# Optimization experiments

Measured on AMD Instinct MI355X. Metric: run time of the kernel, lower is better.

## Reference

```python
import jax, jax.numpy as jnp
import numpy as np

NUM_VARS = 10
HID = 256
INP = 4
B = 32
T = 64

_adj = np.ones((NUM_VARS, NUM_VARS)) - np.eye(NUM_VARS)
SEND, RECV = np.where(_adj)          # each [E], E = num_vars*(num_vars-1) = 90
E = len(SEND)
_e2n = np.zeros((NUM_VARS, E), dtype=np.float32)
_e2n[RECV, np.arange(E)] = 1.0       # encode_onehot(recv).T -> [num_vars, E]
E2N = jnp.asarray(_e2n)
SEND_J = jnp.asarray(SEND)
RECV_J = jnp.asarray(RECV)


def _mlp_block(x, w1, b1, w2, b2, gamma, beta):
    # RefNRIMLP: elu(fc1) -> (dropout p=0) -> elu(fc2) -> batchnorm over view(-1, H)
    h = jax.nn.elu(x @ w1 + b1)
    h = jax.nn.elu(h @ w2 + b2)
    mu = h.mean(axis=(0, 1, 2), keepdims=True)
    var = h.var(axis=(0, 1, 2), keepdims=True)
    return gamma * (h - mu) * jax.lax.rsqrt(var + 1e-5) + beta


def setup_inputs() -> dict:
    key = jax.random.key(0)
    ks = jax.random.split(key, 12)

    def xavier(k, fi, fo):
        return jax.random.normal(k, (fi, fo), jnp.float32) * np.sqrt(2.0 / (fi + fo))

    d = {
        "x": jax.random.normal(ks[0], (B, T, NUM_VARS, INP), jnp.float32),
        # mlp1: inp -> hid -> hid
        "w1a": xavier(ks[1], INP, HID), "b1a": jnp.full((HID,), 0.1),
        "w1b": xavier(ks[2], HID, HID), "b1b": jnp.full((HID,), 0.1),
        "g1": jnp.ones((HID,)), "be1": jnp.zeros((HID,)),
        # mlp2: 2*hid -> hid -> hid
        "w2a": xavier(ks[3], 2 * HID, HID), "b2a": jnp.full((HID,), 0.1),
        "w2b": xavier(ks[4], HID, HID), "b2b": jnp.full((HID,), 0.1),
        "g2": jnp.ones((HID,)), "be2": jnp.zeros((HID,)),
        # mlp3: hid -> hid -> hid
        "w3a": xavier(ks[5], HID, HID), "b3a": jnp.full((HID,), 0.1),
        "w3b": xavier(ks[6], HID, HID), "b3b": jnp.full((HID,), 0.1),
        "g3": jnp.ones((HID,)), "be3": jnp.zeros((HID,)),
        # output heads
        "wo1": xavier(ks[7], HID, HID), "bo1": jnp.full((HID,), 0.1),
        "wo2": xavier(ks[8], HID, 1), "bo2": jnp.full((1,), 0.1),
    }
    return d


def reference(x, w1a, b1a, w1b, b1b, g1, be1,
              w2a, b2a, w2b, b2b, g2, be2,
              w3a, b3a, w3b, b3b, g3, be3,
              wo1, bo1, wo2, bo2):
    # x: [B, T, N, INP] -> transpose(2,1): [B, N, T, INP]
    h = jnp.transpose(x, (0, 2, 1, 3))
    h = _mlp_block(h, w1a, b1a, w1b, b1b, g1, be1)            # [B, N, T, H]
    # node2edge: gather senders/receivers along node dim, concat on features
    e = jnp.concatenate([h[:, SEND_J], h[:, RECV_J]], axis=-1)  # [B, E, T, 2H]
    e = _mlp_block(e, w2a, b2a, w2b, b2b, g2, be2)            # [B, E, T, H]
    # edge2node: incidence matmul over edge dim, normalize by in-degree
    n = jnp.einsum('ve,betH->bvtH', E2N, e) / (NUM_VARS - 1)   # [B, N, T, H]
    n = _mlp_block(n, w3a, b3a, w3b, b3b, g3, be3)
    n = jax.nn.relu(n) @ wo1 + bo1
    n = jax.nn.relu(n) @ wo2 + bo2                             # [B, N, T, 1]
    out = jnp.transpose(n, (0, 2, 1, 3)).mean(axis=-1)         # [B, T, N]
    return out
```

## Files before the change

### kernel.cpp

```cpp
#include <hip/hip_runtime.h>
#include <hip/hip_bf16.h>
#include <cstdint>

#define DI __device__ __forceinline__

typedef short bf16x8 __attribute__((ext_vector_type(8)));
typedef float f32x4 __attribute__((ext_vector_type(4)));
typedef unsigned short u16;
typedef unsigned short u16x8 __attribute__((ext_vector_type(8)));

static constexpr int NV = 10, NE = 90, TT = 64;
static constexpr int R1 = 20480;
static constexpr int R2 = 184320;

DI float bf2f(u16 u) { union { unsigned int i; float f; } x; x.i = ((unsigned int)u) << 16; return x.f; }
DI u16 f2bf(float f) { unsigned int u = __float_as_uint(f); return (u16)((u + 0x7FFF + ((u >> 16) & 1)) >> 16); }
DI float elu(float v) { return v > 0.f ? v : __expf(v) - 1.f; }

#define GLL(srcp, dstp) __builtin_amdgcn_global_load_lds( \
    (const __attribute__((address_space(1))) unsigned int*)(srcp), \
    (__attribute__((address_space(3))) unsigned int*)(dstp), 16, 0, 0)

__global__ __launch_bounds__(256) void pack4(
    const float* __restrict__ s0, u16* __restrict__ d0,
    const float* __restrict__ s1, u16* __restrict__ d1,
    const float* __restrict__ s2, u16* __restrict__ d2,
    const float* __restrict__ s3, u16* __restrict__ d3) {
    const float* s; u16* d;
    switch (blockIdx.y) {
        case 0: s = s0; d = d0; break;
        case 1: s = s1; d = d1; break;
        case 2: s = s2; d = d2; break;
        default: s = s3; d = d3; break;
    }
    int tid = threadIdx.x;
    int bn = blockIdx.x >> 3, kt = blockIdx.x & 7;
#pragma unroll
    for (int p = 0; p < 2; ++p) {
        int n = bn * 128 + p * 64 + (tid >> 2);
        int k = kt * 32 + (tid & 3) * 8;
        u16x8 pk;
#pragma unroll
        for (int e = 0; e < 8; ++e) pk[e] = f2bf(s[(size_t)(k + e) * 256 + n]);
        *(u16x8*)(d + ((size_t)((bn * 8 + kt) * 2 + p)) * 2048 + (size_t)tid * 8) = pk;
    }
}

__global__ __launch_bounds__(256) void pack256s(const float* __restrict__ s,
                                                u16* __restrict__ d) {
    int kt = blockIdx.x;
#pragma unroll
    for (int h = 0; h < 4; ++h) {
        int tid2 = threadIdx.x + h * 256;
        int n = tid2 >> 2;
        int g = (tid2 & 3) ^ ((tid2 >> 2) & 3);
        int k = kt * 32 + g * 8;
        u16x8 pk;
#pragma unroll
        for (int e = 0; e < 8; ++e) pk[e] = f2bf(s[(size_t)(k + e) * 256 + n]);
        *(u16x8*)(d + (size_t)kt * 8192 + (size_t)tid2 * 8) = pk;
    }
}

__global__ __launch_bounds__(256) void pack256s_w2a(const float* __restrict__ w2a,
                                                    const float* __restrict__ scsh1,
                                                    u16* __restrict__ d) {
    int kt = blockIdx.x;
#pragma unroll
    for (int h = 0; h < 4; ++h) {
        int tid2 = threadIdx.x + h * 256;
        int n = tid2 >> 2;
        int g = (tid2 & 3) ^ ((tid2 >> 2) & 3);
        int k = kt * 32 + g * 8;
        u16x8 pk;
#pragma unroll
        for (int e = 0; e < 8; ++e)
            pk[e] = f2bf(scsh1[(k + e) & 255] * w2a[(size_t)(k + e) * 256 + n]);
        *(u16x8*)(d + (size_t)kt * 8192 + (size_t)tid2 * 8) = pk;
    }
}

__global__ void zero_stats(float* p, int n) {
    int i = blockIdx.x * 256 + threadIdx.x;
    if (i < n) p[i] = 0.f;
}

__global__ void conv_wo2(const float* __restrict__ src, u16* __restrict__ dst) {
    dst[threadIdx.x] = f2bf(src[threadIdx.x]);
}

__global__ __launch_bounds__(256) void fold_b2a(const float* __restrict__ w2a,
                                                const float* __restrict__ scsh1,
                                                const float* __restrict__ b2a,
                                                float* __restrict__ b2aF) {
    __shared__ float red[256];
    int n = blockIdx.x, tid = threadIdx.x;
    float sc = scsh1[256 + tid];
    float s = sc * w2a[tid * 256 + n] + sc * w2a[(tid + 256) * 256 + n];
    red[tid] = s;
    __syncthreads();
    for (int off2 = 128; off2 > 0; off2 >>= 1) {
        if (tid < off2) red[tid] += red[tid + off2];
        __syncthreads();
    }
    if (tid == 0) b2aF[n] = red[0] + b2a[n];
}

__global__ void stats_final(const float* __restrict__ sums, const float* __restrict__ g,
                            const float* __restrict__ be, float invR, float* __restrict__ scsh) {
    int c = threadIdx.x;
    float mu = sums[c] * invR;
    float var = sums[256 + c] * invR - mu * mu;
    float rs = rsqrtf(var + 1e-5f);
    float sc = g[c] * rs;
    scsh[c] = sc;
    scsh[256 + c] = be[c] - mu * sc;
}

__global__ __launch_bounds__(256) void mlp1_fc1(const float* __restrict__ x,
                                                const float* __restrict__ w1a,
                                                const float* __restrict__ b1a,
                                                u16* __restrict__ ha) {
    int tid = threadIdx.x;
    int row = blockIdx.x * 8 + (tid >> 5);
    int ch8 = (tid & 31) * 8;
    int b = row / (NV * TT);
    int v = (row >> 6) % NV;
    int t = row & 63;
    const float* xp = x + ((size_t)(b * TT + t) * NV + v) * 4;
    float x0 = xp[0], x1 = xp[1], x2 = xp[2], x3 = xp[3];
    u16x8 pack;
#pragma unroll
    for (int e = 0; e < 8; ++e) {
        int c = ch8 + e;
        float acc = b1a[c] + x0 * w1a[c] + x1 * w1a[256 + c] + x2 * w1a[512 + c] + x3 * w1a[768 + c];
        pack[e] = f2bf(elu(acc));
    }
    *(u16x8*)(ha + (size_t)row * 256 + ch8) = pack;
}

template <int ACT, bool STATS>
__global__ __launch_bounds__(256) void gemm_kernel(const u16* __restrict__ A,
                                                   const u16* __restrict__ Wt,
                                                   const float* __restrict__ bias,
                                                   u16* __restrict__ out,
                                                   int K,
                                                   float* __restrict__ stats) {
    __shared__ u16 As[3][128 * 32];
    __shared__ u16 Bs[3][128 * 32];
    const int tid = threadIdx.x;
    const int lane = tid & 63, wid = tid >> 6;

    int bm, bn;
    {
        int bid = blockIdx.x;
        int xcd = bid & 7, slot = bid >> 3;
        bn = slot & 1;
        bm = xcd + 8 * (slot >> 1);
    }
    const int m0 = bm * 128, n0 = bn * 128;
    const int wm = wid >> 1, wn = wid & 1;

    const int srow = tid >> 2;
    const int scol8 = (tid & 3) * 8;

    size_t abase0 = (size_t)(m0 + srow) * K;
    size_t abase1 = (size_t)(m0 + srow + 64) * K;
    const int NT = K >> 5;
    const size_t bnbase = (size_t)bn * NT * 4096;

    f32x4 acc[4][4];
#pragma unroll
    for (int i = 0; i < 4; ++i)
#pragma unroll
        for (int j = 0; j < 4; ++j) acc[i][j] = (f32x4)0.f;

    const int lrow = lane & 15;
    const int lk8 = (lane >> 4) * 8;

    auto stage = [&](int bf, int k0) {
        const size_t btile = bnbase + (size_t)(k0 >> 5) * 4096 + (size_t)tid * 8;
        GLL(A + abase0 + k0 + scol8, &As[bf][(wid * 64) * 8]);
        GLL(Wt + btile, &Bs[bf][(wid * 64) * 8]);
        GLL(A + abase1 + k0 + scol8, &As[bf][(256 + wid * 64) * 8]);
        GLL(Wt + btile + 2048, &Bs[bf][(256 + wid * 64) * 8]);
    };

    stage(0, 0);
    stage(1, 32);
    for (int kt = 0; kt < NT; ++kt) {
        if (kt + 1 < NT) {
            asm volatile("s_waitcnt vmcnt(4)" ::: "memory");
        } else {
            asm volatile("s_waitcnt vmcnt(0)" ::: "memory");
        }
        __builtin_amdgcn_s_barrier();
        if (kt + 2 < NT) stage((kt + 2) % 3, (kt + 2) * 32);
        __builtin_amdgcn_sched_barrier(0);
        const int buf = kt % 3;
        bf16x8 a[4], b[4];
#pragma unroll
        for (int i = 0; i < 4; ++i)
            a[i] = *(const bf16x8*)&As[buf][(wm * 64 + i * 16 + lrow) * 32 + lk8];
#pragma unroll
        for (int j = 0; j < 4; ++j)
            b[j] = *(const bf16x8*)&Bs[buf][(wn * 64 + j * 16 + lrow) * 32 + lk8];
#pragma unroll
        for (int i = 0; i < 4; ++i)
#pragma unroll
            for (int j = 0; j < 4; ++j)
                acc[i][j] = __builtin_amdgcn_mfma_f32_16x16x32_bf16(a[i], b[j], acc[i][j], 0, 0, 0);
    }

    float bv[4], sv[4], qv[4];
#pragma unroll
    for (int j = 0; j < 4; ++j) {
        bv[j] = bias[n0 + wn * 64 + j * 16 + lrow];
        if constexpr (STATS) { sv[j] = 0.f; qv[j] = 0.f; }
    }
#pragma unroll
    for (int i = 0; i < 4; ++i) {
#pragma unroll
        for (int j = 0; j < 4; ++j) {
            int col = n0 + wn * 64 + j * 16 + lrow;
#pragma unroll
            for (int r = 0; r < 4; ++r) {
                int row = m0 + wm * 64 + i * 16 + (lane >> 4) * 4 + r;
                float v = acc[i][j][r] + bv[j];
                v = (ACT == 1) ? elu(v) : (v > 0.f ? v : 0.f);
                if constexpr (STATS) { sv[j] += v; qv[j] += v * v; }
                out[(size_t)row * 256 + col] = f2bf(v);
            }
        }
    }
    if constexpr (STATS) {
#pragma unroll
        for (int j = 0; j < 4; ++j) {
            float s = sv[j], q_ = qv[j];
            s += __shfl_xor(s, 16); q_ += __shfl_xor(q_, 16);
            s += __shfl_xor(s, 32); q_ += __shfl_xor(q_, 32);
            if ((lane >> 4) == 0) {
                int col = n0 + wn * 64 + j * 16 + lrow;
                atomicAdd(&stats[col], s);
                atomicAdd(&stats[256 + col], q_);
            }
        }
    }
}

__global__ __launch_bounds__(512) void mlp2_fused(const u16* __restrict__ A,
                                                  const u16* __restrict__ PB1,
                                                  const float* __restrict__ bias1,
                                                  const u16* __restrict__ PB2,
                                                  const float* __restrict__ bias2,
                                                  u16* __restrict__ out,
                                                  float* __restrict__ stats) {
    __shared__ u16 As[3][128 * 32];
    __shared__ u16 Bs[3][256 * 32];
    __shared__ u16 H1[128 * 256];

    const int tid = threadIdx.x;
    const int lane = tid & 63, wid = tid >> 6;

    int bid = blockIdx.x;
    int xcd = bid & 7, slot = bid >> 3;
    int batch = xcd + 8 * (slot / 45);
    int bm = batch * 45 + (slot % 45);
    const int m0 = bm * 128;
    const int wm = wid >> 2, wn = wid & 3;

    size_t sb, rb;
    {
        int m = m0 + (tid >> 2);
        int t = m & 63, be = m >> 6, e = be % NE, b = be / NE;
        int s = e / 9, kk = e - s * 9, r = kk + (kk >= s ? 1 : 0);
        int achk = (tid & 3) ^ ((tid >> 2) & 3);
        sb = ((size_t)((b * NV + s) * TT + t)) * 256 + achk * 8;
        rb = ((size_t)((b * NV + r) * TT + t)) * 256 + achk * 8;
    }

    const int lrow = lane & 15;
    const int lsw = (((lane >> 4) ^ (lrow & 3))) * 8;

    f32x4 acc[4][4];
#pragma unroll
    for (int i = 0; i < 4; ++i)
#pragma unroll
        for (int j = 0; j < 4; ++j) acc[i][j] = (f32x4)0.f;

    auto stage1 = [&](int bf, int k0) {
        GLL(A + (k0 < 256 ? sb : rb) + (k0 & 255), &As[bf][tid * 8]);
        const u16* b_ = PB1 + (size_t)(k0 >> 5) * 8192 + (size_t)tid * 8;
        GLL(b_, &Bs[bf][tid * 8]);
        GLL(b_ + 4096, &Bs[bf][4096 + tid * 8]);
    };
    auto stage2 = [&](int bf, int k0) {
        const u16* b_ = PB2 + (size_t)(k0 >> 5) * 8192 + (size_t)tid * 8;
        GLL(b_, &Bs[bf][tid * 8]);
        GLL(b_ + 4096, &Bs[bf][4096 + tid * 8]);
    };

    stage1(0, 0);
    stage1(1, 32);
    for (int kt = 0; kt < 16; ++kt) {
        if (kt + 1 < 16) {
            asm volatile("s_waitcnt vmcnt(3)" ::: "memory");
        } else {
            asm volatile("s_waitcnt vmcnt(0)" ::: "memory");
        }
        __builtin_amdgcn_s_barrier();
        if (kt + 2 < 16) stage1((kt + 2) % 3, (kt + 2) * 32);
        __builtin_amdgcn_sched_barrier(0);
        const int buf = kt % 3;
        bf16x8 a[4], b[4];
#pragma unroll
        for (int i = 0; i < 4; ++i)
            a[i] = *(const bf16x8*)&As[buf][(wm * 64 + i * 16 + lrow) * 32 + lsw];
#pragma unroll
        for (int j = 0; j < 4; ++j)
            b[j] = *(const bf16x8*)&Bs[buf][(wn * 64 + j * 16 + lrow) * 32 + lsw];
#pragma unroll
        for (int i = 0; i < 4; ++i)
#pragma unroll
            for (int j = 0; j < 4; ++j)
                acc[i][j] = __builtin_amdgcn_mfma_f32_16x16x32_bf16(a[i], b[j], acc[i][j], 0, 0, 0);
    }

    __builtin_amdgcn_s_barrier();
    stage2(0, 0);
    stage2(1, 32);
    __builtin_amdgcn_sched_barrier(0);

#pragma unroll
    for (int j = 0; j < 4; ++j) {
        int c = wn * 64 + j * 16 + lrow;
        float bv = bias1[c];
        int gx = c >> 3;
        int cl = c & 7;
#pragma unroll
        for (int i = 0; i < 4; ++i) {
#pragma unroll
            for (int r = 0; r < 4; ++r) {
                int m = wm * 64 + i * 16 + (lane >> 4) * 4 + r;
                float v = elu(acc[i][j][r] + bv);
                H1[m * 256 + ((gx ^ (m & 7)) << 3) + cl] = f2bf(v);
            }
        }
    }
    __syncthreads();

#pragma unroll
    for (int i = 0; i < 4; ++i)
#pragma unroll
        for (int j = 0; j < 4; ++j) acc[i][j] = (f32x4)0.f;

    for (int kt = 0; kt < 8; ++kt) {
        if (kt + 1 < 8) {
            asm volatile("s_waitcnt vmcnt(2)" ::: "memory");
        } else {
            asm volatile("s_waitcnt vmcnt(0)" ::: "memory");
        }
        __builtin_amdgcn_s_barrier();
        if (kt + 2 < 8) stage2((kt + 2) % 3, (kt + 2) * 32);
        __builtin_amdgcn_sched_barrier(0);
        const int buf = kt % 3;
        const int k0 = kt * 32;
        bf16x8 a[4], b[4];
#pragma unroll
        for (int i = 0; i < 4; ++i) {
            int mr = wm * 64 + i * 16 + lrow;
            int gx = (k0 >> 3) + (lane >> 4);
            a[i] = *(const bf16x8*)&H1[mr * 256 + ((gx ^ (mr & 7)) << 3)];
        }
#pragma unroll
        for (int j = 0; j < 4; ++j)
            b[j] = *(const bf16x8*)&Bs[buf][(wn * 64 + j * 16 + lrow) * 32 + lsw];
#pragma unroll
        for (int i = 0; i < 4; ++i)
#pragma unroll
            for (int j = 0; j < 4; ++j)
                acc[i][j] = __builtin_amdgcn_mfma_f32_16x16x32_bf16(a[i], b[j], acc[i][j], 0, 0, 0);
    }

    float bv2[4], sv[4], qv[4];
#pragma unroll
    for (int j = 0; j < 4; ++j) {
        bv2[j] = bias2[wn * 64 + j * 16 + lrow];
        sv[j] = 0.f;
        qv[j] = 0.f;
    }
#pragma unroll
    for (int i = 0; i < 4; ++i) {
#pragma unroll
        for (int j = 0; j < 4; ++j) {
            int col = wn * 64 + j * 16 + lrow;
#pragma unroll
            for (int r = 0; r < 4; ++r) {
                int row = m0 + wm * 64 + i * 16 + (lane >> 4) * 4 + r;
                float v = elu(acc[i][j][r] + bv2[j]);
                sv[j] += v;
                qv[j] += v * v;
                out[(size_t)row * 256 + col] = f2bf(v);
            }
        }
    }
#pragma unroll
    for (int j = 0; j < 4; ++j) {
        float s = sv[j], q_ = qv[j];
        s += __shfl_xor(s, 16); q_ += __shfl_xor(q_, 16);
        s += __shfl_xor(s, 32); q_ += __shfl_xor(q_, 32);
        if ((lane >> 4) == 0) {
            int col = wn * 64 + j * 16 + lrow;
            atomicAdd(&stats[col], s);
            atomicAdd(&stats[256 + col], q_);
        }
    }
}

__global__ __launch_bounds__(256) void norm_affine_relu(const u16* __restrict__ in,
                                                        const float* __restrict__ scsh,
                                                        u16* __restrict__ out, int n8) {
    int i = blockIdx.x * 256 + threadIdx.x;
    if (i >= n8) return;
    size_t base = (size_t)i * 8;
    int ch8 = (int)(base & 255);
    u16x8 v = *(const u16x8*)(in + base);
    u16x8 o;
#pragma unroll
    for (int e = 0; e < 8; ++e) {
        float f = bf2f(v[e]);
        f = scsh[ch8 + e] * f + scsh[256 + ch8 + e];
        o[e] = f2bf(f > 0.f ? f : 0.f);
    }
    *(u16x8*)(out + base) = o;
}

__global__ __launch_bounds__(256) void edge2node(const u16* __restrict__ h2,
                                                 const float* __restrict__ scsh2,
                                                 u16* __restrict__ n1) {
    int tid = threadIdx.x;
    int row = blockIdx.x * 8 + (tid >> 5);
    int ch8 = (tid & 31) * 8;
    int t = row & 63;
    int bv = row >> 6;
    int v = bv % NV;
    int b = bv / NV;
    float acc[8] = {0, 0, 0, 0, 0, 0, 0, 0};
#pragma unroll
    for (int i = 0; i < 9; ++i) {
        int s = i + (i >= v ? 1 : 0);
        int e = s * 9 + (v < s ? v : v - 1);
        u16x8 vv = *(const u16x8*)(h2 + ((size_t)((b * NE + e) * TT + t)) * 256 + ch8);
#pragma unroll
        for (int k = 0; k < 8; ++k) acc[k] += bf2f(vv[k]);
    }
    const float inv9 = 1.f / 9.f;
    u16x8 o;
#pragma unroll
    for (int k = 0; k < 8; ++k) {
        int c = ch8 + k;
        o[k] = f2bf(scsh2[c] * (acc[k] * inv9) + scsh2[256 + c]);
    }
    *(u16x8*)(n1 + (size_t)row * 256 + ch8) = o;
}

__global__ __launch_bounds__(256) void head2(const u16* __restrict__ a2,
                                             const u16* __restrict__ wo2t,
                                             const float* __restrict__ bo2,
                                             float* __restrict__ out) {
    int tid = threadIdx.x;
    int row = blockIdx.x * 8 + (tid >> 5);
    int l32 = tid & 31;
    int ch8 = l32 * 8;
    u16x8 a = *(const u16x8*)(a2 + (size_t)row * 256 + ch8);
    u16x8 w = *(const u16x8*)(wo2t + ch8);
    float p = 0.f;
#pragma unroll
    for (int k = 0; k < 8; ++k) p += bf2f(a[k]) * bf2f(w[k]);
#pragma unroll
    for (int off = 16; off > 0; off >>= 1) p += __shfl_down(p, off, 32);
    if (l32 == 0) {
        int b = row / (NV * TT);
        int v = (row >> 6) % NV;
        int t = row & 63;
        out[(size_t)(b * TT + t) * NV + v] = p + bo2[0];
    }
}

extern "C" void kernel_launch(void* const* d_in, const int* in_sizes, int n_in,
                              void* d_out, int out_size, void* d_ws, size_t ws_size,
                              hipStream_t stream) {
    const float* x   = (const float*)d_in[0];
    const float* w1a = (const float*)d_in[1];
    const float* b1a = (const float*)d_in[2];
    const float* w1b = (const float*)d_in[3];
    const float* b1b = (const float*)d_in[4];
    const float* g1  = (const float*)d_in[5];
    const float* be1 = (const float*)d_in[6];
    const float* w2a = (const float*)d_in[7];
    const float* b2a = (const float*)d_in[8];
    const float* w2b = (const float*)d_in[9];
    const float* b2b = (const float*)d_in[10];
    const float* g2  = (const float*)d_in[11];
    const float* be2 = (const float*)d_in[12];
    const float* w3a = (const float*)d_in[13];
    const float* b3a = (const float*)d_in[14];
    const float* w3b = (const float*)d_in[15];
    const float* b3b = (const float*)d_in[16];
    const float* g3  = (const float*)d_in[17];
    const float* be3 = (const float*)d_in[18];
    const float* wo1 = (const float*)d_in[19];
    const float* bo1 = (const float*)d_in[20];
    const float* wo2 = (const float*)d_in[21];
    const float* bo2 = (const float*)d_in[22];
    float* out = (float*)d_out;

    char* ws = (char*)d_ws;
    size_t off = 0;
    auto alloc = [&](size_t bytes) {
        void* p = ws + off;
        off = (off + bytes + 255) & ~(size_t)255;
        return p;
    };
    u16* w1bP = (u16*)alloc(2 * 8 * 4096 * 2);
    u16* w3aP = (u16*)alloc(2 * 8 * 4096 * 2);
    u16* w3bP = (u16*)alloc(2 * 8 * 4096 * 2);
    u16* wo1P = (u16*)alloc(2 * 8 * 4096 * 2);
    u16* w2aP = (u16*)alloc(16 * 8192 * 2);
    u16* w2bP = (u16*)alloc(8 * 8192 * 2);
    u16* wo2T = (u16*)alloc(256 * 2);
    float* sums  = (float*)alloc(3 * 512 * 4);
    float* scsh1 = (float*)alloc(512 * 4);
    float* scsh2 = (float*)alloc(512 * 4);
    float* scsh3 = (float*)alloc(512 * 4);
    float* b2aF  = (float*)alloc(256 * 4);
    u16* S0 = (u16*)alloc((size_t)R1 * 256 * 2);
    u16* S1 = (u16*)alloc((size_t)R1 * 256 * 2);
    u16* S2 = (u16*)alloc((size_t)R1 * 256 * 2);
    u16* BIG2 = (u16*)alloc((size_t)R2 * 256 * 2);

    dim3 pgrid(16, 4);
    pack4<<<pgrid, 256, 0, stream>>>(w1b, w1bP, w3a, w3aP, w3b, w3bP, wo1, wo1P);
    pack256s<<<8, 256, 0, stream>>>(w2b, w2bP);
    zero_stats<<<6, 256, 0, stream>>>(sums, 3 * 512);
    conv_wo2<<<1, 256, 0, stream>>>(wo2, wo2T);

    mlp1_fc1<<<R1 / 8, 256, 0, stream>>>(x, w1a, b1a, S0);
    gemm_kernel<1, true><<<(R1 / 128) * 2, 256, 0, stream>>>(S0, w1bP, b1b, S1, 256, sums);
    stats_final<<<1, 256, 0, stream>>>(sums, g1, be1, 1.f / R1, scsh1);
    pack256s_w2a<<<16, 256, 0, stream>>>(w2a, scsh1, w2aP);
    fold_b2a<<<256, 256, 0, stream>>>(w2a, scsh1, b2a, b2aF);

    mlp2_fused<<<R2 / 128, 512, 0, stream>>>(S1, w2aP, b2aF, w2bP, b2b, BIG2, sums + 512);
    stats_final<<<1, 256, 0, stream>>>(sums + 512, g2, be2, 1.f / R2, scsh2);

    edge2node<<<R1 / 8, 256, 0, stream>>>(BIG2, scsh2, S0);

    gemm_kernel<1, false><<<(R1 / 128) * 2, 256, 0, stream>>>(S0, w3aP, b3a, S1, 256, nullptr);
    gemm_kernel<1, true><<<(R1 / 128) * 2, 256, 0, stream>>>(S1, w3bP, b3b, S2, 256, sums + 1024);
    stats_final<<<1, 256, 0, stream>>>(sums + 1024, g3, be3, 1.f / R1, scsh3);

    norm_affine_relu<<<(R1 * 32 + 255) / 256, 256, 0, stream>>>(S2, scsh3, S0, R1 * 32);
    gemm_kernel<2, false><<<(R1 / 128) * 2, 256, 0, stream>>>(S0, wo1P, bo1, S1, 256, nullptr);
    head2<<<R1 / 8, 256, 0, stream>>>(S1, wo2T, bo2, out);
}
```

Before: 249.4 us.

## Fuse mlp3 GEMM pair and output head, inline BN stats finalization

Adds an mlp3_fused kernel that keeps the elu(fc1) activations in shared memory and runs fc2 in the same block. It also adds a head_fused kernel that computes the wo1 GEMM, relu, and the wo2 dot product with an in-block reduction. The stats_final launches are removed, with consumers recomputing scale and shift from the raw sums, and w3a/w3b/wo1 are repacked into a 256-wide layout. This cuts several kernel launches and the global round-trips of intermediates. The cost is some redundant per-element rsqrt work and smaller 64-row tiles.

```diff
diff --git a/kernel.cpp b/kernel.cpp
--- a/kernel.cpp
+++ b/kernel.cpp
@@ -12,6 +12,8 @@
 static constexpr int NV = 10, NE = 90, TT = 64;
 static constexpr int R1 = 20480;
 static constexpr int R2 = 184320;
+static constexpr float INV_R1 = 1.f / 20480.f;
+static constexpr float INV_R2 = 1.f / 184320.f;
 
 DI float bf2f(u16 u) { union { unsigned int i; float f; } x; x.i = ((unsigned int)u) << 16; return x.f; }
 DI u16 f2bf(float f) { unsigned int u = __float_as_uint(f); return (u16)((u + 0x7FFF + ((u >> 16) & 1)) >> 16); }
@@ -21,28 +23,41 @@
     (const __attribute__((address_space(1))) unsigned int*)(srcp), \
     (__attribute__((address_space(3))) unsigned int*)(dstp), 16, 0, 0)
 
-__global__ __launch_bounds__(256) void pack4(
+__global__ __launch_bounds__(256) void pack128(const float* __restrict__ s,
+                                               u16* __restrict__ d) {
+    int tid = threadIdx.x;
+    int bn = blockIdx.x >> 3, kt = blockIdx.x & 7;
+#pragma unroll
+    for (int p = 0; p < 2; ++p) {
+        int n = bn * 128 + p * 64 + (tid >> 2);
+        int k = kt * 32 + (tid & 3) * 8;
+        u16x8 pk;
+#pragma unroll
+        for (int e = 0; e < 8; ++e) pk[e] = f2bf(s[(size_t)(k + e) * 256 + n]);
+        *(u16x8*)(d + ((size_t)((bn * 8 + kt) * 2 + p)) * 2048 + (size_t)tid * 8) = pk;
+    }
+}
+
+__global__ __launch_bounds__(256) void pack256_3(
     const float* __restrict__ s0, u16* __restrict__ d0,
     const float* __restrict__ s1, u16* __restrict__ d1,
-    const float* __restrict__ s2, u16* __restrict__ d2,
-    const float* __restrict__ s3, u16* __restrict__ d3) {
+    const float* __restrict__ s2, u16* __restrict__ d2) {
     const float* s; u16* d;
     switch (blockIdx.y) {
         case 0: s = s0; d = d0; break;
         case 1: s = s1; d = d1; break;
-        case 2: s = s2; d = d2; break;
-        default: s = s3; d = d3; break;
-    }
-    int tid = threadIdx.x;
-    int bn = blockIdx.x >> 3, kt = blockIdx.x & 7;
-#pragma unroll
-    for (int p = 0; p < 2; ++p) {
-        int n = bn * 128 + p * 64 + (tid >> 2);
-        int k = kt * 32 + (tid & 3) * 8;
+        default: s = s2; d = d2; break;
+    }
+    int kt = blockIdx.x;
+#pragma unroll
+    for (int h = 0; h < 4; ++h) {
+        int tid2 = threadIdx.x + h * 256;
+        int n = tid2 >> 2;
+        int k = kt * 32 + (tid2 & 3) * 8;
         u16x8 pk;
 #pragma unroll
         for (int e = 0; e < 8; ++e) pk[e] = f2bf(s[(size_t)(k + e) * 256 + n]);
-        *(u16x8*)(d + ((size_t)((bn * 8 + kt) * 2 + p)) * 2048 + (size_t)tid * 8) = pk;
+        *(u16x8*)(d + (size_t)kt * 8192 + (size_t)tid2 * 8) = pk;
     }
 }
 
@@ -63,7 +78,8 @@
 }
 
 __global__ __launch_bounds__(256) void pack256s_w2a(const float* __restrict__ w2a,
-                                                    const float* __restrict__ scsh1,
+                                                    const float* __restrict__ sums,
+                                                    const float* __restrict__ g1,
                                                     u16* __restrict__ d) {
     int kt = blockIdx.x;
 #pragma unroll
@@ -74,8 +90,13 @@
         int k = kt * 32 + g * 8;
         u16x8 pk;
 #pragma unroll
-        for (int e = 0; e < 8; ++e)
-            pk[e] = f2bf(scsh1[(k + e) & 255] * w2a[(size_t)(k + e) * 256 + n]);
+        for (int e = 0; e < 8; ++e) {
+            int c = (k + e) & 255;
+            float mu = sums[c] * INV_R1;
+            float var = sums[256 + c] * INV_R1 - mu * mu;
+            float sc = g1[c] * rsqrtf(var + 1e-5f);
+            pk[e] = f2bf(sc * w2a[(size_t)(k + e) * 256 + n]);
+        }
         *(u16x8*)(d + (size_t)kt * 8192 + (size_t)tid2 * 8) = pk;
     }
 }
@@ -85,18 +106,19 @@
     if (i < n) p[i] = 0.f;
 }
 
-__global__ void conv_wo2(const float* __restrict__ src, u16* __restrict__ dst) {
-    dst[threadIdx.x] = f2bf(src[threadIdx.x]);
-}
-
 __global__ __launch_bounds__(256) void fold_b2a(const float* __restrict__ w2a,
-                                                const float* __restrict__ scsh1,
+                                                const float* __restrict__ sums,
+                                                const float* __restrict__ g1,
+                                                const float* __restrict__ be1,
                                                 const float* __restrict__ b2a,
                                                 float* __restrict__ b2aF) {
     __shared__ float red[256];
     int n = blockIdx.x, tid = threadIdx.x;
-    float sc = scsh1[256 + tid];
-    float s = sc * w2a[tid * 256 + n] + sc * w2a[(tid + 256) * 256 + n];
+    float mu = sums[tid] * INV_R1;
+    float var = sums[256 + tid] * INV_R1 - mu * mu;
+    float sc = g1[tid] * rsqrtf(var + 1e-5f);
+    float sh = be1[tid] - mu * sc;
+    float s = sh * w2a[tid * 256 + n] + sh * w2a[(tid + 256) * 256 + n];
     red[tid] = s;
     __syncthreads();
     for (int off2 = 128; off2 > 0; off2 >>= 1) {
@@ -104,17 +126,6 @@
         __syncthreads();
     }
     if (tid == 0) b2aF[n] = red[0] + b2a[n];
-}
-
-__global__ void stats_final(const float* __restrict__ sums, const float* __restrict__ g,
-                            const float* __restrict__ be, float invR, float* __restrict__ scsh) {
-    int c = threadIdx.x;
-    float mu = sums[c] * invR;
-    float var = sums[256 + c] * invR - mu * mu;
-    float rs = rsqrtf(var + 1e-5f);
-    float sc = g[c] * rs;
-    scsh[c] = sc;
-    scsh[256 + c] = be[c] - mu * sc;
 }
 
 __global__ __launch_bounds__(256) void mlp1_fc1(const float* __restrict__ x,
@@ -417,8 +428,264 @@
     }
 }
 
+__global__ __launch_bounds__(256) void mlp3_fused(const u16* __restrict__ A,
+                                                  const u16* __restrict__ PB1,
+                                                  const float* __restrict__ bias1,
+                                                  const u16* __restrict__ PB2,
+                                                  const float* __restrict__ bias2,
+                                                  u16* __restrict__ out,
+                                                  float* __restrict__ stats) {
+    __shared__ u16 As[2][64 * 32];
+    __shared__ u16 Bs[2][256 * 32];
+    __shared__ u16 H1[64 * 256];
+
+    const int tid = threadIdx.x;
+    const int lane = tid & 63, wid = tid >> 6;
+    int bid = blockIdx.x;
+    int bm = (bid & 7) * 40 + (bid >> 3);
+    const int m0 = bm * 64;
+    const int wn = wid;
+
+    const size_t ab = (size_t)(m0 + (tid >> 2)) * 256 + (tid & 3) * 8;
+
+    const int lrow = lane & 15;
+    const int lk8 = (lane >> 4) * 8;
+
+    f32x4 acc[4][4];
+#pragma unroll
+    for (int i = 0; i < 4; ++i)
+#pragma unroll
+        for (int j = 0; j < 4; ++j) acc[i][j] = (f32x4)0.f;
+
+    auto stage1 = [&](int bf, int k0) {
+        GLL(A + ab + k0, &As[bf][tid * 8]);
+        const u16* b_ = PB1 + (size_t)(k0 >> 5) * 8192;
+#pragma unroll
+        for (int q = 0; q < 4; ++q)
+            GLL(b_ + (q * 256 + tid) * 8, &Bs[bf][(q * 256 + tid) * 8]);
+    };
+    auto stage2 = [&](int bf, int k0) {
+        const u16* b_ = PB2 + (size_t)(k0 >> 5) * 8192;
+#pragma unroll
+        for (int q = 0; q < 4; ++q)
+            GLL(b_ + (q * 256 + tid) * 8, &Bs[bf][(q * 256 + tid) * 8]);
+    };
+
+    stage1(0, 0);
+    __syncthreads();
+    for (int kt = 0; kt < 8; ++kt) {
+        if (kt + 1 < 8) stage1((kt + 1) & 1, (kt + 1) * 32);
+        const int buf = kt & 1;
+        bf16x8 a[4], b[4];
+#pragma unroll
+        for (int i = 0; i < 4; ++i)
+            a[i] = *(const bf16x8*)&As[buf][(i * 16 + lrow) * 32 + lk8];
+#pragma unroll
+        for (int j = 0; j < 4; ++j)
+            b[j] = *(const bf16x8*)&Bs[buf][(wn * 64 + j * 16 + lrow) * 32 + lk8];
+#pragma unroll
+        for (int i = 0; i < 4; ++i)
+#pragma unroll
+            for (int j = 0; j < 4; ++j)
+                acc[i][j] = __builtin_amdgcn_mfma_f32_16x16x32_bf16(a[i], b[j], acc[i][j], 0, 0, 0);
+        __syncthreads();
+    }
+
+    stage2(0, 0);
+    __builtin_amdgcn_sched_barrier(0);
+
+#pragma unroll
+    for (int j = 0; j < 4; ++j) {
+        int c = wn * 64 + j * 16 + lrow;
+        float bv = bias1[c];
+        int gx = c >> 3;
+        int cl = c & 7;
+#pragma unroll
+        for (int i = 0; i < 4; ++i) {
+#pragma unroll
+            for (int r = 0; r < 4; ++r) {
+                int m = i * 16 + (lane >> 4) * 4 + r;
+                float v = elu(acc[i][j][r] + bv);
+                H1[m * 256 + ((gx ^ (m & 7)) << 3) + cl] = f2bf(v);
+            }
+        }
+    }
+    __syncthreads();
+
+#pragma unroll
+    for (int i = 0; i < 4; ++i)
+#pragma unroll
+        for (int j = 0; j < 4; ++j) acc[i][j] = (f32x4)0.f;
+
+    for (int kt = 0; kt < 8; ++kt) {
+        if (kt + 1 < 8) stage2((kt + 1) & 1, (kt + 1) * 32);
+        const int buf = kt & 1;
+        const int k0 = kt * 32;
+        bf16x8 a[4], b[4];
+#pragma unroll
+        for (int i = 0; i < 4; ++i) {
+            int mr = i * 16 + lrow;
+            int gx = (k0 >> 3) + (lane >> 4);
+            a[i] = *(const bf16x8*)&H1[mr * 256 + ((gx ^ (mr & 7)) << 3)];
+        }
+#pragma unroll
+        for (int j = 0; j < 4; ++j)
+            b[j] = *(const bf16x8*)&Bs[buf][(wn * 64 + j * 16 + lrow) * 32 + lk8];
+#pragma unroll
+        for (int i = 0; i < 4; ++i)
+#pragma unroll
+            for (int j = 0; j < 4; ++j)
+                acc[i][j] = __builtin_amdgcn_mfma_f32_16x16x32_bf16(a[i], b[j], acc[i][j], 0, 0, 0);
+        __syncthreads();
+    }
+
+    float bv2[4], sv[4], qv[4];
+#pragma unroll
+    for (int j = 0; j < 4; ++j) {
+        bv2[j] = bias2[wn * 64 + j * 16 + lrow];
+        sv[j] = 0.f;
+        qv[j] = 0.f;
+    }
+#pragma unroll
+    for (int i = 0; i < 4; ++i) {
+#pragma unroll
+        for (int j = 0; j < 4; ++j) {
+            int col = wn * 64 + j * 16 + lrow;
+#pragma unroll
+            for (int r = 0; r < 4; ++r) {
+                int row = m0 + i * 16 + (lane >> 4) * 4 + r;
+                float v = elu(acc[i][j][r] + bv2[j]);
+                sv[j] += v;
+                qv[j] += v * v;
+                out[(size_t)row * 256 + col] = f2bf(v);
+            }
+        }
+    }
+#pragma unroll
+    for (int j = 0; j < 4; ++j) {
+        float s = sv[j], q_ = qv[j];
+        s += __shfl_xor(s, 16); q_ += __shfl_xor(q_, 16);
+        s += __shfl_xor(s, 32); q_ += __shfl_xor(q_, 32);
+        if ((lane >> 4) == 0) {
+            int col = wn * 64 + j * 16 + lrow;
+            atomicAdd(&stats[col], s);
+            atomicAdd(&stats[256 + col], q_);
+        }
+    }
+}
+
+__global__ __launch_bounds__(256) void head_fused(const u16* __restrict__ A,
+                                                  const u16* __restrict__ PB1,
+                                                  const float* __restrict__ bo1,
+                                                  const float* __restrict__ wo2,
+                                                  const float* __restrict__ bo2,
+                                                  float* __restrict__ out) {
+    __shared__ u16 As[2][64 * 32];
+    __shared__ u16 Bs[2][256 * 32];
+    __shared__ float rs[64 * 4];
+
+    const int tid = threadIdx.x;
+    const int lane = tid & 63, wid = tid >> 6;
+    int bid = blockIdx.x;
+    int bm = (bid & 7) * 40 + (bid >> 3);
+    const int m0 = bm * 64;
+    const int wn = wid;
+
+    const size_t ab = (size_t)(m0 + (tid >> 2)) * 256 + (tid & 3) * 8;
+
+    const int lrow = lane & 15;
+    const int lk8 = (lane >> 4) * 8;
+
+    f32x4 acc[4][4];
+#pragma unroll
+    for (int i = 0; i < 4; ++i)
+#pragma unroll
+        for (int j = 0; j < 4; ++j) acc[i][j] = (f32x4)0.f;
+
+    auto stage1 = [&](int bf, int k0) {
+        GLL(A + ab + k0, &As[bf][tid * 8]);
+        const u16* b_ = PB1 + (size_t)(k0 >> 5) * 8192;
+#pragma unroll
+        for (int q = 0; q < 4; ++q)
+            GLL(b_ + (q * 256 + tid) * 8, &Bs[bf][(q * 256 + tid) * 8]);
+    };
+
+    stage1(0, 0);
+    __syncthreads();
+    for (int kt = 0; kt < 8; ++kt) {
+        if (kt + 1 < 8) stage1((kt + 1) & 1, (kt + 1) * 32);
+        const int buf = kt & 1;
+        bf16x8 a[4], b[4];
+#pragma unroll
+        for (int i = 0; i < 4; ++i)
+            a[i] = *(const bf16x8*)&As[buf][(i * 16 + lrow) * 32 + lk8];
+#pragma unroll
+        for (int j = 0; j < 4; ++j)
+            b[j] = *(const bf16x8*)&Bs[buf][(wn * 64 + j * 16 + lrow) * 32 + lk8];
+#pragma unroll
+        for (int i = 0; i < 4; ++i)
+#pragma unroll
+            for (int j = 0; j < 4; ++j)
+                acc[i][j] = __builtin_amdgcn_mfma_f32_16x16x32_bf16(a[i], b[j], acc[i][j], 0, 0, 0);
+        __syncthreads();
+    }
+
+    float p[4][4];
+#pragma unroll
+    for (int i = 0; i < 4; ++i)
+#pragma unroll
+        for (int r = 0; r < 4; ++r) p[i][r] = 0.f;
+#pragma unroll
+    for (int j = 0; j < 4; ++j) {
+        int col = wn * 64 + j * 16 + lrow;
+        float bv = bo1[col];
+        float w = wo2[col];
+#pragma unroll
+        for (int i = 0; i < 4; ++i) {
+#pragma unroll
+            for (int r = 0; r < 4; ++r) {
+                float v = acc[i][j][r] + bv;
+                v = v > 0.f ? v : 0.f;
+                p[i][r] += v * w;
+            }
+        }
+    }
+#pragma unroll
+    for (int i = 0; i < 4; ++i) {
+#pragma unroll
+        for (int r = 0; r < 4; ++r) {
+            float s = p[i][r];
+            s += __shfl_xor(s, 1);
+            s += __shfl_xor(s, 2);
+            s += __shfl_xor(s, 4);
+            s += __shfl_xor(s, 8);
+            p[i][r] = s;
+        }
+    }
+    if (lrow == 0) {
+#pragma unroll
+        for (int i = 0; i < 4; ++i)
+#pragma unroll
+            for (int r = 0; r < 4; ++r) {
+                int rowlocal = i * 16 + (lane >> 4) * 4 + r;
+                rs[rowlocal * 4 + wn] = p[i][r];
+            }
+    }
+    __syncthreads();
+    if (tid < 64) {
+        float s = rs[tid * 4] + rs[tid * 4 + 1] + rs[tid * 4 + 2] + rs[tid * 4 + 3] + bo2[0];
+        int m = m0 + tid;
+        int b = m / (NV * TT);
+        int v = (m >> 6) % NV;
+        int t = m & 63;
+        out[(size_t)(b * TT + t) * NV + v] = s;
+    }
+}
+
 __global__ __launch_bounds__(256) void norm_affine_relu(const u16* __restrict__ in,
-                                                        const float* __restrict__ scsh,
+                                                        const float* __restrict__ sums,
+                                                        const float* __restrict__ g3,
+                                                        const float* __restrict__ be3,
                                                         u16* __restrict__ out, int n8) {
     int i = blockIdx.x * 256 + threadIdx.x;
     if (i >= n8) return;
@@ -428,15 +695,21 @@
     u16x8 o;
 #pragma unroll
     for (int e = 0; e < 8; ++e) {
-        float f = bf2f(v[e]);
-        f = scsh[ch8 + e] * f + scsh[256 + ch8 + e];
+        int c = ch8 + e;
+        float mu = sums[c] * INV_R1;
+        float var = sums[256 + c] * INV_R1 - mu * mu;
+        float sc = g3[c] * rsqrtf(var + 1e-5f);
+        float sh = be3[c] - mu * sc;
+        float f = bf2f(v[e]) * sc + sh;
         o[e] = f2bf(f > 0.f ? f : 0.f);
     }
     *(u16x8*)(out + base) = o;
 }
 
 __global__ __launch_bounds__(256) void edge2node(const u16* __restrict__ h2,
-                                                 const float* __restrict__ scsh2,
+                                                 const float* __restrict__ sums,
+                                                 const float* __restrict__ g2,
+                                                 const float* __restrict__ be2,
                                                  u16* __restrict__ n1) {
     int tid = threadIdx.x;
     int row = blockIdx.x * 8 + (tid >> 5);
@@ -459,32 +732,13 @@
 #pragma unroll
     for (int k = 0; k < 8; ++k) {
         int c = ch8 + k;
-        o[k] = f2bf(scsh2[c] * (acc[k] * inv9) + scsh2[256 + c]);
+        float mu = sums[c] * INV_R2;
+        float var = sums[256 + c] * INV_R2 - mu * mu;
+        float sc = g2[c] * rsqrtf(var + 1e-5f);
+        float sh = be2[c] - mu * sc;
+        o[k] = f2bf(sc * (acc[k] * inv9) + sh);
     }
     *(u16x8*)(n1 + (size_t)row * 256 + ch8) = o;
-}
-
-__global__ __launch_bounds__(256) void head2(const u16* __restrict__ a2,
-                                             const u16* __restrict__ wo2t,
-                                             const float* __restrict__ bo2,
-                                             float* __restrict__ out) {
-    int tid = threadIdx.x;
-    int row = blockIdx.x * 8 + (tid >> 5);
-    int l32 = tid & 31;
-    int ch8 = l32 * 8;
-    u16x8 a = *(const u16x8*)(a2 + (size_t)row * 256 + ch8);
-    u16x8 w = *(const u16x8*)(wo2t + ch8);
-    float p = 0.f;
-#pragma unroll
-    for (int k = 0; k < 8; ++k) p += bf2f(a[k]) * bf2f(w[k]);
-#pragma unroll
-    for (int off = 16; off > 0; off >>= 1) p += __shfl_down(p, off, 32);
-    if (l32 == 0) {
-        int b = row / (NV * TT);
-        int v = (row >> 6) % NV;
-        int t = row & 63;
-        out[(size_t)(b * TT + t) * NV + v] = p + bo2[0];
-    }
 }
 
 extern "C" void kernel_launch(void* const* d_in, const int* in_sizes, int n_in,
@@ -523,44 +777,35 @@
         return p;
     };
     u16* w1bP = (u16*)alloc(2 * 8 * 4096 * 2);
-    u16* w3aP = (u16*)alloc(2 * 8 * 4096 * 2);
-    u16* w3bP = (u16*)alloc(2 * 8 * 4096 * 2);
-    u16* wo1P = (u16*)alloc(2 * 8 * 4096 * 2);
+    u16* w3aP = (u16*)alloc(8 * 8192 * 2);
+    u16* w3bP = (u16*)alloc(8 * 8192 * 2);
+    u16* wo1P = (u16*)alloc(8 * 8192 * 2);
     u16* w2aP = (u16*)alloc(16 * 8192 * 2);
     u16* w2bP = (u16*)alloc(8 * 8192 * 2);
-    u16* wo2T = (u16*)alloc(256 * 2);
     float* sums  = (float*)alloc(3 * 512 * 4);
-    float* scsh1 = (float*)alloc(512 * 4);
-    float* scsh2 = (float*)alloc(512 * 4);
-    float* scsh3 = (float*)alloc(512 * 4);
     float* b2aF  = (float*)alloc(256 * 4);
     u16* S0 = (u16*)alloc((size_t)R1 * 256 * 2);
     u16* S1 = (u16*)alloc((size_t)R1 * 256 * 2);
     u16* S2 = (u16*)alloc((size_t)R1 * 256 * 2);
     u16* BIG2 = (u16*)alloc((size_t)R2 * 256 * 2);
 
-    dim3 pgrid(16, 4);
-    pack4<<<pgrid, 256, 0, stream>>>(w1b, w1bP, w3a, w3aP, w3b, w3bP, wo1, wo1P);
+    pack128<<<16, 256, 0, stream>>>(w1b, w1bP);
+    dim3 p3grid(8, 3);
+    pack256_3<<<p3grid, 256, 0, stream>>>(w3a, w3aP, w3b, w3bP, wo1, wo1P);
     pack256s<<<8, 256, 0, stream>>>(w2b, w2bP);
     zero_stats<<<6, 256, 0, stream>>>(sums, 3 * 512);
-    conv_wo2<<<1, 256, 0, stream>>>(wo2, wo2T);
 
     mlp1_fc1<<<R1 / 8, 256, 0, stream>>>(x, w1a, b1a, S0);
     gemm_kernel<1, true><<<(R1 / 128) * 2, 256, 0, stream>>>(S0, w1bP, b1b, S1, 256, sums);
-    stats_final<<<1, 256, 0, stream>>>(sums, g1, be1, 1.f / R1, scsh1);
-    pack256s_w2a<<<16, 256, 0, stream>>>(w2a, scsh1, w2aP);
-    fold_b2a<<<256, 256, 0, stream>>>(w2a, scsh1, b2a, b2aF);
+    pack256s_w2a<<<16, 256, 0, stream>>>(w2a, sums, g1, w2aP);
+    fold_b2a<<<256, 256, 0, stream>>>(w2a, sums, g1, be1, b2a, b2aF);
 
     mlp2_fused<<<R2 / 128, 512, 0, stream>>>(S1, w2aP, b2aF, w2bP, b2b, BIG2, sums + 512);
-    stats_final<<<1, 256, 0, stream>>>(sums + 512, g2, be2, 1.f / R2, scsh2);
-
-    edge2node<<<R1 / 8, 256, 0, stream>>>(BIG2, scsh2, S0);
-
-    gemm_kernel<1, false><<<(R1 / 128) * 2, 256, 0, stream>>>(S0, w3aP, b3a, S1, 256, nullptr);
-    gemm_kernel<1, true><<<(R1 / 128) * 2, 256, 0, stream>>>(S1, w3bP, b3b, S2, 256, sums + 1024);
-    stats_final<<<1, 256, 0, stream>>>(sums + 1024, g3, be3, 1.f / R1, scsh3);
-
-    norm_affine_relu<<<(R1 * 32 + 255) / 256, 256, 0, stream>>>(S2, scsh3, S0, R1 * 32);
-    gemm_kernel<2, false><<<(R1 / 128) * 2, 256, 0, stream>>>(S0, wo1P, bo1, S1, 256, nullptr);
-    head2<<<R1 / 8, 256, 0, stream>>>(S1, wo2T, bo2, out);
-}
+
+    edge2node<<<R1 / 8, 256, 0, stream>>>(BIG2, sums + 512, g2, be2, S0);
+
+    mlp3_fused<<<R1 / 64, 256, 0, stream>>>(S0, w3aP, b3a, w3bP, b3b, S2, sums + 1024);
+
+    norm_affine_relu<<<(R1 * 32 + 255) / 256, 256, 0, stream>>>(S2, sums + 1024, g3, be3, S0, R1 * 32);
+    head_fused<<<R1 / 64, 256, 0, stream>>>(S0, wo1P, bo1, wo2, bo2, out);
+}
```

After: 239.3 us (median of 2 runs). 4.1% less time.
